# Optimization experiments

Hardware: AMD Instinct MI355X
Metric: run time of the kernel (lower is better)

## Reference

```python
import jax, jax.numpy as jnp
import numpy as np

N_NODES = 50000
N_EDGES = 800000
IN_DIM = 64
HID = 128
HEADS = 4
C = HID // HEADS  # per-head channels
NUM_CLASSES = 2
NEG_SLOPE = 0.2
LN_EPS = 1e-5


def _glorot(key, shape, fan_in):
    return jax.random.normal(key, shape, dtype=jnp.float32) * (1.0 / np.sqrt(fan_in))


def setup_inputs() -> dict:
    key = jax.random.key(0)
    ks = jax.random.split(key, 32)
    x = jax.random.normal(ks[0], (N_NODES, IN_DIM), dtype=jnp.float32)
    edge_index = jax.random.randint(ks[1], (2, N_EDGES), 0, N_NODES, dtype=jnp.int64)
    inp = {"x": x, "edge_index": edge_index}
    # GATConv 1 (in_dim -> heads*C, concat)
    inp["W1"] = _glorot(ks[2], (IN_DIM, HEADS * C), IN_DIM)
    inp["as1"] = _glorot(ks[3], (HEADS, C), C)
    inp["ad1"] = _glorot(ks[4], (HEADS, C), C)
    inp["b1"] = jnp.zeros((HID,), jnp.float32)
    inp["g1"] = jnp.ones((HID,), jnp.float32)
    inp["be1"] = jnp.zeros((HID,), jnp.float32)
    # residual projection in_dim -> hidden
    inp["rw"] = _glorot(ks[5], (IN_DIM, HID), IN_DIM)
    inp["rb"] = jnp.zeros((HID,), jnp.float32)
    # GATConv 2
    inp["W2"] = _glorot(ks[6], (HID, HEADS * C), HID)
    inp["as2"] = _glorot(ks[7], (HEADS, C), C)
    inp["ad2"] = _glorot(ks[8], (HEADS, C), C)
    inp["b2"] = jnp.zeros((HID,), jnp.float32)
    inp["g2"] = jnp.ones((HID,), jnp.float32)
    inp["be2"] = jnp.zeros((HID,), jnp.float32)
    # GATConv 3
    inp["W3"] = _glorot(ks[9], (HID, HEADS * C), HID)
    inp["as3"] = _glorot(ks[10], (HEADS, C), C)
    inp["ad3"] = _glorot(ks[11], (HEADS, C), C)
    inp["b3"] = jnp.zeros((HID,), jnp.float32)
    inp["g3"] = jnp.ones((HID,), jnp.float32)
    inp["be3"] = jnp.zeros((HID,), jnp.float32)
    # output GATConv (hidden -> num_classes, heads=1, concat=False)
    inp["Wo"] = _glorot(ks[12], (HID, NUM_CLASSES), HID)
    inp["aso"] = _glorot(ks[13], (1, NUM_CLASSES), NUM_CLASSES)
    inp["ado"] = _glorot(ks[14], (1, NUM_CLASSES), NUM_CLASSES)
    inp["bo"] = jnp.zeros((NUM_CLASSES,), jnp.float32)
    return inp


def gat_conv(x, src, dst, W, a_src, a_dst, bias, heads, c, concat):
    """PyG GATConv (add_self_loops=True, negative_slope=0.2, eval-mode dropout)."""
    N = x.shape[0]
    xl = (x @ W).reshape(N, heads, c)                       # [N,H,C]
    al_s = jnp.einsum("nhc,hc->nh", xl, a_src)               # [N,H]
    al_d = jnp.einsum("nhc,hc->nh", xl, a_dst)               # [N,H]
    loop = jnp.arange(N, dtype=src.dtype)
    s = jnp.concatenate([src, loop])                          # [E+N]
    d = jnp.concatenate([dst, loop])
    e = jax.nn.leaky_relu(al_s[s] + al_d[d], NEG_SLOPE)       # [E+N,H]
    m = jax.ops.segment_max(e, d, num_segments=N)             # per-dst max
    e = jnp.exp(e - m[d])
    denom = jax.ops.segment_sum(e, d, num_segments=N)
    alpha = e / (denom[d] + 1e-16)                            # [E+N,H]
    msg = xl[s] * alpha[:, :, None]                           # [E+N,H,C]
    out = jax.ops.segment_sum(msg, d, num_segments=N)         # [N,H,C]
    if concat:
        return out.reshape(N, heads * c) + bias
    return out.mean(axis=1) + bias


def layer_norm(x, g, b):
    mu = jnp.mean(x, axis=-1, keepdims=True)
    var = jnp.mean((x - mu) ** 2, axis=-1, keepdims=True)
    return (x - mu) * jax.lax.rsqrt(var + LN_EPS) * g + b


def reference(x, edge_index, W1, as1, ad1, b1, g1, be1, rw, rb,
              W2, as2, ad2, b2, g2, be2, W3, as3, ad3, b3, g3, be3,
              Wo, aso, ado, bo):
    src, dst = edge_index[0], edge_index[1]
    res = x @ rw + rb
    h = gat_conv(x, src, dst, W1, as1, ad1, b1, HEADS, C, True)
    h = jax.nn.relu(layer_norm(h, g1, be1)) + res
    res = h
    h2 = gat_conv(h, src, dst, W2, as2, ad2, b2, HEADS, C, True)
    h = jax.nn.relu(layer_norm(h2, g2, be2)) + res
    res = h
    h3 = gat_conv(h, src, dst, W3, as3, ad3, b3, HEADS, C, True)
    h = jax.nn.relu(layer_norm(h3, g3, be3)) + res
    out = gat_conv(h, src, dst, Wo, aso, ado, bo, 1, NUM_CLASSES, False)
    return out
```

## Files before the change

### kernel.cpp

```cpp
#include <hip/hip_runtime.h>
#include <math.h>

#define HID 128
#define HEADS 4
#define NEG_SLOPE 0.2f
#define LN_EPS 1e-5f
#define BCAP 4096

typedef unsigned short ushortT;
typedef unsigned int uintT;
typedef __attribute__((ext_vector_type(8))) short bf16x8;
typedef __attribute__((ext_vector_type(4))) float f32x4;

__device__ __forceinline__ float lrelu(float v) { return v > 0.f ? v : NEG_SLOPE * v; }
__device__ __forceinline__ float bflo(uintT v) { return __uint_as_float(v << 16); }
__device__ __forceinline__ float bfhi(uintT v) { return __uint_as_float(v & 0xffff0000u); }

__device__ __forceinline__ ushortT f2bf(float f) {
    uintT u = __float_as_uint(f);
    u += 0x7fffu + ((u >> 16) & 1u);
    return (ushortT)(u >> 16);
}

__global__ __launch_bounds__(256) void binA_k(const int* __restrict__ src, const int* __restrict__ dst,
                                              int* __restrict__ gcur, int2* __restrict__ buf, int E, int NB) {
    __shared__ int hist[512];
    __shared__ int bbase[512];
    __shared__ int lcur[512];
    int t = threadIdx.x;
    for (int i = t; i < NB; i += 256) { hist[i] = 0; lcur[i] = 0; }
    __syncthreads();
    int e0 = blockIdx.x * 4096;
    int2 ed[16];
    #pragma unroll
    for (int j = 0; j < 16; ++j) {
        int idx = e0 + j * 256 + t;
        if (idx < E) {
            ed[j].x = src[idx];
            ed[j].y = dst[idx];
            atomicAdd(&hist[ed[j].y >> 7], 1);
        } else {
            ed[j].y = -1;
        }
    }
    __syncthreads();
    for (int i = t; i < NB; i += 256) {
        int c = hist[i];
        bbase[i] = c > 0 ? atomicAdd(&gcur[i], c) : 0;
    }
    __syncthreads();
    #pragma unroll
    for (int j = 0; j < 16; ++j) {
        if (ed[j].y >= 0) {
            int b = ed[j].y >> 7;
            int pos = bbase[b] + atomicAdd(&lcur[b], 1);
            buf[(size_t)b * BCAP + pos] = ed[j];
        }
    }
}

__global__ __launch_bounds__(64) void scanB_k(const int* __restrict__ bcnt, int* __restrict__ bbase, int NB) {
    int t = threadIdx.x;
    int carry = 0;
    for (int base = 0; base < NB; base += 64) {
        int idx = base + t;
        int v = idx < NB ? bcnt[idx] : 0;
        int inc = v;
        #pragma unroll
        for (int ofs = 1; ofs < 64; ofs <<= 1) {
            int p = __shfl_up(inc, ofs, 64);
            if (t >= ofs) inc += p;
        }
        if (idx < NB) bbase[idx] = carry + inc - v;
        carry += __shfl(inc, 63, 64);
    }
}

__global__ __launch_bounds__(256) void binB_k(const int2* __restrict__ buf, const int* __restrict__ bcnt,
                                              const int* __restrict__ bbase, int* __restrict__ off,
                                              int* __restrict__ csr, int Nn, int E) {
    __shared__ int cnt[128];
    __shared__ int pre[128];
    __shared__ int cur[128];
    int t = threadIdx.x, b = blockIdx.x;
    if (t < 128) cnt[t] = 0;
    __syncthreads();
    int nb = bcnt[b];
    int base = bbase[b];
    int nodebase = b << 7;
    for (int i = t; i < nb; i += 256)
        atomicAdd(&cnt[buf[(size_t)b * BCAP + i].y - nodebase], 1);
    __syncthreads();
    if (t < 128) pre[t] = cnt[t];
    __syncthreads();
    #pragma unroll
    for (int ofs = 1; ofs < 128; ofs <<= 1) {
        int v = 0;
        if (t < 128 && t >= ofs) v = pre[t - ofs];
        __syncthreads();
        if (t < 128) pre[t] += v;
        __syncthreads();
    }
    if (t < 128) {
        int node = nodebase + t;
        int o = base + pre[t] - cnt[t];
        if (node < Nn) off[node] = o;
        cur[t] = o;
    }
    if (b == 0 && t == 0) off[Nn] = E;
    __syncthreads();
    for (int i = t; i < nb; i += 256) {
        int2 e = buf[(size_t)b * BCAP + i];
        int p = atomicAdd(&cur[e.y - nodebase], 1);
        csr[p] = e.x;
    }
}

__global__ __launch_bounds__(256) void wconv4_k(const float* __restrict__ rw, const float* __restrict__ W1,
                                                const float* __restrict__ W2, const float* __restrict__ W3,
                                                ushortT* __restrict__ rwf, ushortT* __restrict__ W1f,
                                                ushortT* __restrict__ W2f, ushortT* __restrict__ W3f) {
    int id = blockIdx.x * 256 + threadIdx.x;
    const float* Wsrc; ushortT* Wdst; int kdiv; int lid;
    if (id < 8192)        { Wsrc = rw; Wdst = rwf; kdiv = 2; lid = id; }
    else if (id < 16384)  { Wsrc = W1; Wdst = W1f; kdiv = 2; lid = id - 8192; }
    else if (id < 32768)  { Wsrc = W2; Wdst = W2f; kdiv = 4; lid = id - 16384; }
    else if (id < 49152)  { Wsrc = W3; Wdst = W3f; kdiv = 4; lid = id - 32768; }
    else return;
    int i = lid & 7;
    int lane = (lid >> 3) & 63;
    int rest = lid >> 9;
    int ks = rest % kdiv;
    int j = rest / kdiv;
    int k = ks * 32 + (lane >> 4) * 8 + i;
    int n = j * 16 + (lane & 15);
    Wdst[lid] = f2bf(Wsrc[k * HID + n]);
}

__global__ __launch_bounds__(256) void gemm_mfma_x(
        const float* __restrict__ X, const ushortT* __restrict__ rwf, const ushortT* __restrict__ W1f,
        const float* __restrict__ rb, const float* __restrict__ a_srcp, const float* __restrict__ a_dstp,
        float* __restrict__ Cres, ushortT* __restrict__ Ch,
        float* __restrict__ als, float* __restrict__ ald, int M) {
    int t = threadIdx.x;
    int wave = t >> 6, lane = t & 63;
    int row0 = blockIdx.x * 64 + wave * 16;
    int cl = lane & 15, grp = lane >> 4;
    int rA = row0 + cl;
    f32x4 accR[8] = {};
    f32x4 acc1[8] = {};
    #pragma unroll
    for (int ks = 0; ks < 2; ++ks) {
        bf16x8 afr = {};
        if (rA < M) {
            const float* xr = &X[(size_t)rA * 64 + ks * 32 + grp * 8];
            float4 a0 = *(const float4*)xr;
            float4 a1 = *(const float4*)(xr + 4);
            afr[0] = (short)f2bf(a0.x); afr[1] = (short)f2bf(a0.y);
            afr[2] = (short)f2bf(a0.z); afr[3] = (short)f2bf(a0.w);
            afr[4] = (short)f2bf(a1.x); afr[5] = (short)f2bf(a1.y);
            afr[6] = (short)f2bf(a1.z); afr[7] = (short)f2bf(a1.w);
        }
        #pragma unroll
        for (int j = 0; j < 8; ++j) {
            bf16x8 br = *(const bf16x8*)&rwf[(((size_t)j * 2 + ks) * 64 + lane) * 8];
            accR[j] = __builtin_amdgcn_mfma_f32_16x16x32_bf16(afr, br, accR[j], 0, 0, 0);
            bf16x8 b1 = *(const bf16x8*)&W1f[(((size_t)j * 2 + ks) * 64 + lane) * 8];
            acc1[j] = __builtin_amdgcn_mfma_f32_16x16x32_bf16(afr, b1, acc1[j], 0, 0, 0);
        }
    }
    float asv[8], adv[8], rbv[8];
    #pragma unroll
    for (int j = 0; j < 8; ++j) {
        asv[j] = a_srcp[j * 16 + cl];
        adv[j] = a_dstp[j * 16 + cl];
        rbv[j] = rb[j * 16 + cl];
    }
    #pragma unroll
    for (int reg = 0; reg < 4; ++reg) {
        int r = row0 + grp * 4 + reg;
        bool ok = r < M;
        if (ok) {
            #pragma unroll
            for (int j = 0; j < 8; ++j) {
                Cres[(size_t)r * HID + j * 16 + cl] = accR[j][reg] + rbv[j];
                Ch[(size_t)r * HID + j * 16 + cl] = f2bf(acc1[j][reg]);
            }
        }
        float ps[4], pd[4];
        #pragma unroll
        for (int h = 0; h < 4; ++h) {
            ps[h] = acc1[2 * h][reg] * asv[2 * h] + acc1[2 * h + 1][reg] * asv[2 * h + 1];
            pd[h] = acc1[2 * h][reg] * adv[2 * h] + acc1[2 * h + 1][reg] * adv[2 * h + 1];
        }
        #pragma unroll
        for (int m = 1; m < 16; m <<= 1) {
            #pragma unroll
            for (int h = 0; h < 4; ++h) {
                ps[h] += __shfl_xor(ps[h], m, 64);
                pd[h] += __shfl_xor(pd[h], m, 64);
            }
        }
        if (cl == 0 && ok) {
            *(float4*)&als[(size_t)r * 4] = make_float4(ps[0], ps[1], ps[2], ps[3]);
            *(float4*)&ald[(size_t)r * 4] = make_float4(pd[0], pd[1], pd[2], pd[3]);
        }
    }
}

__global__ __launch_bounds__(256) void gemm_mfma_h(
        const ushortT* __restrict__ Ah, const ushortT* __restrict__ Wf,
        const float* __restrict__ a_srcp, const float* __restrict__ a_dstp,
        ushortT* __restrict__ Ch, float* __restrict__ als, float* __restrict__ ald, int M) {
    int t = threadIdx.x;
    int wave = t >> 6, lane = t & 63;
    int row0 = blockIdx.x * 64 + wave * 16;
    int cl = lane & 15, grp = lane >> 4;
    int rA = row0 + cl;
    f32x4 acc[8] = {};
    #pragma unroll
    for (int ks = 0; ks < 4; ++ks) {
        bf16x8 afr = {};
        if (rA < M) afr = *(const bf16x8*)&Ah[(size_t)rA * HID + ks * 32 + grp * 8];
        #pragma unroll
        for (int j = 0; j < 8; ++j) {
            bf16x8 br = *(const bf16x8*)&Wf[(((size_t)j * 4 + ks) * 64 + lane) * 8];
            acc[j] = __builtin_amdgcn_mfma_f32_16x16x32_bf16(afr, br, acc[j], 0, 0, 0);
        }
    }
    float asv[8], adv[8];
    #pragma unroll
    for (int j = 0; j < 8; ++j) {
        asv[j] = a_srcp[j * 16 + cl];
        adv[j] = a_dstp[j * 16 + cl];
    }
    #pragma unroll
    for (int reg = 0; reg < 4; ++reg) {
        int r = row0 + grp * 4 + reg;
        bool ok = r < M;
        if (ok) {
            #pragma unroll
            for (int j = 0; j < 8; ++j)
                Ch[(size_t)r * HID + j * 16 + cl] = f2bf(acc[j][reg]);
        }
        float ps[4], pd[4];
        #pragma unroll
        for (int h = 0; h < 4; ++h) {
            ps[h] = acc[2 * h][reg] * asv[2 * h] + acc[2 * h + 1][reg] * asv[2 * h + 1];
            pd[h] = acc[2 * h][reg] * adv[2 * h] + acc[2 * h + 1][reg] * adv[2 * h + 1];
        }
        #pragma unroll
        for (int m = 1; m < 16; m <<= 1) {
            #pragma unroll
            for (int h = 0; h < 4; ++h) {
                ps[h] += __shfl_xor(ps[h], m, 64);
                pd[h] += __shfl_xor(pd[h], m, 64);
            }
        }
        if (cl == 0 && ok) {
            *(float4*)&als[(size_t)r * 4] = make_float4(ps[0], ps[1], ps[2], ps[3]);
            *(float4*)&ald[(size_t)r * 4] = make_float4(pd[0], pd[1], pd[2], pd[3]);
        }
    }
}

__global__ __launch_bounds__(256) void gat_fused(
        const ushortT* __restrict__ xlh, const float* __restrict__ als,
        const float* __restrict__ ald, const int* __restrict__ off,
        const int* __restrict__ csr, const float* __restrict__ bias,
        const float* __restrict__ g, const float* __restrict__ be,
        float* __restrict__ hres, ushortT* __restrict__ hresh,
        const float* __restrict__ Wo, const float* __restrict__ aso, const float* __restrict__ ado,
        float* __restrict__ xlo, float* __restrict__ alsoB, float* __restrict__ aldoB, int Nn) {
    int gid = blockIdx.x * 256 + threadIdx.x;
    int wid = gid >> 6, lane = threadIdx.x & 63;
    if (wid >= Nn) return;
    int q = lane >> 4;
    int cl = lane & 15;
    int h = cl >> 2;
    float aldh = ald[wid * 4 + h];
    float eh = lrelu(als[wid * 4 + h] + aldh);
    int b = off[wid], e = off[wid + 1];
    float acc[8] = {};
    float dsum = 0.f;
    int c = b + q;
    for (; c + 4 < e; c += 8) {
        int s0 = csr[c];
        int s1 = csr[c + 4];
        float al0 = als[(size_t)s0 * 4 + h];
        float al1 = als[(size_t)s1 * 4 + h];
        uint4 hv0 = *(const uint4*)&xlh[(size_t)s0 * HID + cl * 8];
        uint4 hv1 = *(const uint4*)&xlh[(size_t)s1 * HID + cl * 8];
        float w0 = __expf(lrelu(al0 + aldh) - eh);
        float w1 = __expf(lrelu(al1 + aldh) - eh);
        dsum += w0 + w1;
        acc[0] = fmaf(w0, bflo(hv0.x), acc[0]);
        acc[1] = fmaf(w0, bfhi(hv0.x), acc[1]);
        acc[2] = fmaf(w0, bflo(hv0.y), acc[2]);
        acc[3] = fmaf(w0, bfhi(hv0.y), acc[3]);
        acc[4] = fmaf(w0, bflo(hv0.z), acc[4]);
        acc[5] = fmaf(w0, bfhi(hv0.z), acc[5]);
        acc[6] = fmaf(w0, bflo(hv0.w), acc[6]);
        acc[7] = fmaf(w0, bfhi(hv0.w), acc[7]);
        acc[0] = fmaf(w1, bflo(hv1.x), acc[0]);
        acc[1] = fmaf(w1, bfhi(hv1.x), acc[1]);
        acc[2] = fmaf(w1, bflo(hv1.y), acc[2]);
        acc[3] = fmaf(w1, bfhi(hv1.y), acc[3]);
        acc[4] = fmaf(w1, bflo(hv1.z), acc[4]);
        acc[5] = fmaf(w1, bfhi(hv1.z), acc[5]);
        acc[6] = fmaf(w1, bflo(hv1.w), acc[6]);
        acc[7] = fmaf(w1, bfhi(hv1.w), acc[7]);
    }
    if (c < e) {
        int s = csr[c];
        float al = als[(size_t)s * 4 + h];
        uint4 hv = *(const uint4*)&xlh[(size_t)s * HID + cl * 8];
        float w = __expf(lrelu(al + aldh) - eh);
        dsum += w;
        acc[0] = fmaf(w, bflo(hv.x), acc[0]);
        acc[1] = fmaf(w, bfhi(hv.x), acc[1]);
        acc[2] = fmaf(w, bflo(hv.y), acc[2]);
        acc[3] = fmaf(w, bfhi(hv.y), acc[3]);
        acc[4] = fmaf(w, bflo(hv.z), acc[4]);
        acc[5] = fmaf(w, bfhi(hv.z), acc[5]);
        acc[6] = fmaf(w, bflo(hv.w), acc[6]);
        acc[7] = fmaf(w, bfhi(hv.w), acc[7]);
    }
    #pragma unroll
    for (int k = 0; k < 8; ++k) {
        acc[k] += __shfl_xor(acc[k], 16, 64);
        acc[k] += __shfl_xor(acc[k], 32, 64);
    }
    dsum += __shfl_xor(dsum, 16, 64);
    dsum += __shfl_xor(dsum, 32, 64);
    float inv = 1.f / (dsum + 1.f + 1e-16f);
    uint4 sv = *(const uint4*)&xlh[(size_t)wid * HID + cl * 8];
    float sx[8];
    sx[0] = bflo(sv.x); sx[1] = bfhi(sv.x);
    sx[2] = bflo(sv.y); sx[3] = bfhi(sv.y);
    sx[4] = bflo(sv.z); sx[5] = bfhi(sv.z);
    sx[6] = bflo(sv.w); sx[7] = bfhi(sv.w);
    float4 bi0 = *(const float4*)&bias[cl * 8];
    float4 bi1 = *(const float4*)&bias[cl * 8 + 4];
    float o[8];
    #pragma unroll
    for (int k = 0; k < 8; ++k) {
        float bb = k < 4 ? (&bi0.x)[k] : (&bi1.x)[k - 4];
        o[k] = fmaf(acc[k] + sx[k], inv, bb);
    }
    float s1 = o[0] + o[1] + o[2] + o[3] + o[4] + o[5] + o[6] + o[7];
    #pragma unroll
    for (int m = 1; m < 16; m <<= 1) s1 += __shfl_xor(s1, m, 64);
    float mu = s1 * (1.0f / HID);
    float qv = 0.f;
    #pragma unroll
    for (int k = 0; k < 8; ++k) { float d = o[k] - mu; qv += d * d; }
    #pragma unroll
    for (int m = 1; m < 16; m <<= 1) qv += __shfl_xor(qv, m, 64);
    float rs = rsqrtf(qv * (1.0f / HID) + LN_EPS);
    if (q == 0) {
        float4 g0 = *(const float4*)&g[cl * 8];
        float4 g1 = *(const float4*)&g[cl * 8 + 4];
        float4 be0 = *(const float4*)&be[cl * 8];
        float4 be1 = *(const float4*)&be[cl * 8 + 4];
        float4 r0 = *(const float4*)&hres[(size_t)wid * HID + cl * 8];
        float4 r1 = *(const float4*)&hres[(size_t)wid * HID + cl * 8 + 4];
        float w[8];
        #pragma unroll
        for (int k = 0; k < 8; ++k) {
            float gg = k < 4 ? (&g0.x)[k] : (&g1.x)[k - 4];
            float ee = k < 4 ? (&be0.x)[k] : (&be1.x)[k - 4];
            float rr = k < 4 ? (&r0.x)[k] : (&r1.x)[k - 4];
            w[k] = fmaxf((o[k] - mu) * rs * gg + ee, 0.f) + rr;
        }
        if (Wo) {
            float p0 = 0.f, p1 = 0.f;
            #pragma unroll
            for (int k = 0; k < 8; ++k) {
                int ch = cl * 8 + k;
                p0 = fmaf(w[k], Wo[ch * 2 + 0], p0);
                p1 = fmaf(w[k], Wo[ch * 2 + 1], p1);
            }
            #pragma unroll
            for (int m = 1; m < 16; m <<= 1) {
                p0 += __shfl_xor(p0, m, 64);
                p1 += __shfl_xor(p1, m, 64);
            }
            if (cl == 0) {
                xlo[wid * 2 + 0] = p0;
                xlo[wid * 2 + 1] = p1;
                alsoB[wid] = p0 * aso[0] + p1 * aso[1];
                aldoB[wid] = p0 * ado[0] + p1 * ado[1];
            }
        } else {
            *(float4*)&hres[(size_t)wid * HID + cl * 8] = make_float4(w[0], w[1], w[2], w[3]);
            *(float4*)&hres[(size_t)wid * HID + cl * 8 + 4] = make_float4(w[4], w[5], w[6], w[7]);
            ushort4 hv0, hv1;
            hv0.x = f2bf(w[0]); hv0.y = f2bf(w[1]); hv0.z = f2bf(w[2]); hv0.w = f2bf(w[3]);
            hv1.x = f2bf(w[4]); hv1.y = f2bf(w[5]); hv1.z = f2bf(w[6]); hv1.w = f2bf(w[7]);
            *(ushort4*)&hresh[(size_t)wid * HID + cl * 8] = hv0;
            *(ushort4*)&hresh[(size_t)wid * HID + cl * 8 + 4] = hv1;
        }
    }
}

__global__ __launch_bounds__(256) void out_agg(const float* __restrict__ xlo, const float* __restrict__ also,
                                               const float* __restrict__ aldo, const int* __restrict__ off,
                                               const int* __restrict__ csr, const float* __restrict__ bo,
                                               float* __restrict__ out, int Nn) {
    int gid = blockIdx.x * 256 + threadIdx.x;
    int wid = gid >> 6, lane = threadIdx.x & 63;
    if (wid >= Nn) return;
    float aldn = aldo[wid];
    float eself = lrelu(also[wid] + aldn);
    int b = off[wid], e = off[wid + 1];
    float dl = 0.f, a0 = 0.f, a1 = 0.f;
    for (int j = b + lane; j < e; j += 64) {
        int s = csr[j];
        float w = __expf(lrelu(also[s] + aldn) - eself);
        dl += w;
        a0 += w * xlo[s * 2 + 0];
        a1 += w * xlo[s * 2 + 1];
    }
    #pragma unroll
    for (int m = 1; m < 64; m <<= 1) {
        dl += __shfl_xor(dl, m, 64);
        a0 += __shfl_xor(a0, m, 64);
        a1 += __shfl_xor(a1, m, 64);
    }
    if (lane == 0) {
        dl += 1.f;
        a0 += xlo[wid * 2 + 0];
        a1 += xlo[wid * 2 + 1];
        float inv = 1.f / (dl + 1e-16f);
        out[wid * 2 + 0] = a0 * inv + bo[0];
        out[wid * 2 + 1] = a1 * inv + bo[1];
    }
}

extern "C" void kernel_launch(void* const* d_in, const int* in_sizes, int n_in,
                              void* d_out, int out_size, void* d_ws, size_t ws_size,
                              hipStream_t stream) {
    const float* x   = (const float*)d_in[0];
    const int*   ei  = (const int*)d_in[1];
    const float* W1  = (const float*)d_in[2];
    const float* as1 = (const float*)d_in[3];
    const float* ad1 = (const float*)d_in[4];
    const float* b1  = (const float*)d_in[5];
    const float* g1  = (const float*)d_in[6];
    const float* be1 = (const float*)d_in[7];
    const float* rw  = (const float*)d_in[8];
    const float* rb  = (const float*)d_in[9];
    const float* W2  = (const float*)d_in[10];
    const float* as2 = (const float*)d_in[11];
    const float* ad2 = (const float*)d_in[12];
    const float* b2  = (const float*)d_in[13];
    const float* g2  = (const float*)d_in[14];
    const float* be2 = (const float*)d_in[15];
    const float* W3  = (const float*)d_in[16];
    const float* as3 = (const float*)d_in[17];
    const float* ad3 = (const float*)d_in[18];
    const float* b3  = (const float*)d_in[19];
    const float* g3  = (const float*)d_in[20];
    const float* be3 = (const float*)d_in[21];
    const float* Wo  = (const float*)d_in[22];
    const float* aso = (const float*)d_in[23];
    const float* ado = (const float*)d_in[24];
    const float* bo  = (const float*)d_in[25];

    int N = in_sizes[0] / 64;
    int E = in_sizes[1] / 2;
    const int* srcE = ei;
    const int* dstE = ei + E;
    int NB = (N + 127) >> 7;

    char* w = (char*)d_ws;
    auto alloc = [&](size_t b) { char* p = w; w += (b + 255) & ~(size_t)255; return p; };
    int* off    = (int*)alloc((size_t)(N + 1) * 4);
    int* gcur   = (int*)alloc((size_t)NB * 4);
    int* bbase  = (int*)alloc((size_t)NB * 4);
    int* csr    = (int*)alloc((size_t)E * 4);
    int2* bbuf  = (int2*)alloc((size_t)NB * BCAP * 8);
    float* hbuf = (float*)alloc((size_t)N * HID * 4);
    ushortT* hresh = (ushortT*)alloc((size_t)N * HID * 2);
    ushortT* xlh = (ushortT*)alloc((size_t)N * HID * 2);
    ushortT* rwf = (ushortT*)alloc(8192 * 2);
    ushortT* W1f = (ushortT*)alloc(8192 * 2);
    ushortT* W2f = (ushortT*)alloc(16384 * 2);
    ushortT* W3f = (ushortT*)alloc(16384 * 2);
    float* als  = (float*)alloc((size_t)N * HEADS * 4);
    float* ald  = (float*)alloc((size_t)N * HEADS * 4);
    float* xlo  = (float*)alloc((size_t)N * 2 * 4);
    float* alsoB = (float*)alloc((size_t)N * 4);
    float* aldoB = (float*)alloc((size_t)N * 4);

    hipMemsetAsync(gcur, 0, (size_t)NB * 4, stream);
    binA_k<<<(E + 4095) / 4096, 256, 0, stream>>>(srcE, dstE, gcur, bbuf, E, NB);
    scanB_k<<<1, 64, 0, stream>>>(gcur, bbase, NB);
    binB_k<<<NB, 256, 0, stream>>>(bbuf, gcur, bbase, off, csr, N, E);

    wconv4_k<<<192, 256, 0, stream>>>(rw, W1, W2, W3, rwf, W1f, W2f, W3f);

    int gG = (N + 63) / 64;
    int gW = (N + 3) / 4;

    gemm_mfma_x<<<gG, 256, 0, stream>>>(x, rwf, W1f, rb, as1, ad1, hbuf, xlh, als, ald, N);
    gat_fused<<<gW, 256, 0, stream>>>(xlh, als, ald, off, csr, b1, g1, be1, hbuf, hresh,
                                      nullptr, nullptr, nullptr, nullptr, nullptr, nullptr, N);

    gemm_mfma_h<<<gG, 256, 0, stream>>>(hresh, W2f, as2, ad2, xlh, als, ald, N);
    gat_fused<<<gW, 256, 0, stream>>>(xlh, als, ald, off, csr, b2, g2, be2, hbuf, hresh,
                                      nullptr, nullptr, nullptr, nullptr, nullptr, nullptr, N);

    gemm_mfma_h<<<gG, 256, 0, stream>>>(hresh, W3f, as3, ad3, xlh, als, ald, N);
    gat_fused<<<gW, 256, 0, stream>>>(xlh, als, ald, off, csr, b3, g3, be3, hbuf, nullptr,
                                      Wo, aso, ado, xlo, alsoB, aldoB, N);

    out_agg<<<gW, 256, 0, stream>>>(xlo, alsoB, aldoB, off, csr, bo, (float*)d_out, N);
}
```

Measured before the change: 244.5 us.

## Store residual in bf16, fold scan and memset, pack output-layer node data

The residual stream is now kept only as bf16 in one buffer that is read and overwritten in place, instead of separate fp32 and bf16 copies. The separate memset and single-block scan kernel are removed: wconv4 zeroes the bucket counters, and each binB block computes its own base by summing the preceding bucket counts. Attention logits are pre-scaled by log2(e) so exp2f can replace __expf. Output-layer per-node values are packed into one float4 so each neighbor costs a single gather. These changes cut launches and memory traffic, at the cost of bf16 rounding in the residual path and redundant prefix sums in binB.

```diff
diff --git a/kernel.cpp b/kernel.cpp
--- a/kernel.cpp
+++ b/kernel.cpp
@@ -5,6 +5,7 @@
 #define HEADS 4
 #define NEG_SLOPE 0.2f
 #define LN_EPS 1e-5f
+#define LOG2E 1.44269504088896f
 #define BCAP 4096
 
 typedef unsigned short ushortT;
@@ -59,34 +60,22 @@
     }
 }
 
-__global__ __launch_bounds__(64) void scanB_k(const int* __restrict__ bcnt, int* __restrict__ bbase, int NB) {
-    int t = threadIdx.x;
-    int carry = 0;
-    for (int base = 0; base < NB; base += 64) {
-        int idx = base + t;
-        int v = idx < NB ? bcnt[idx] : 0;
-        int inc = v;
-        #pragma unroll
-        for (int ofs = 1; ofs < 64; ofs <<= 1) {
-            int p = __shfl_up(inc, ofs, 64);
-            if (t >= ofs) inc += p;
-        }
-        if (idx < NB) bbase[idx] = carry + inc - v;
-        carry += __shfl(inc, 63, 64);
-    }
-}
-
 __global__ __launch_bounds__(256) void binB_k(const int2* __restrict__ buf, const int* __restrict__ bcnt,
-                                              const int* __restrict__ bbase, int* __restrict__ off,
-                                              int* __restrict__ csr, int Nn, int E) {
+                                              int* __restrict__ off, int* __restrict__ csr, int Nn, int E) {
     __shared__ int cnt[128];
     __shared__ int pre[128];
     __shared__ int cur[128];
+    __shared__ int sbase;
     int t = threadIdx.x, b = blockIdx.x;
+    if (t == 0) sbase = 0;
     if (t < 128) cnt[t] = 0;
     __syncthreads();
+    int bacc = 0;
+    for (int i = t; i < b; i += 256) bacc += bcnt[i];
+    #pragma unroll
+    for (int m = 1; m < 64; m <<= 1) bacc += __shfl_xor(bacc, m, 64);
+    if ((t & 63) == 0 && bacc != 0) atomicAdd(&sbase, bacc);
     int nb = bcnt[b];
-    int base = bbase[b];
     int nodebase = b << 7;
     for (int i = t; i < nb; i += 256)
         atomicAdd(&cnt[buf[(size_t)b * BCAP + i].y - nodebase], 1);
@@ -103,7 +92,7 @@
     }
     if (t < 128) {
         int node = nodebase + t;
-        int o = base + pre[t] - cnt[t];
+        int o = sbase + pre[t] - cnt[t];
         if (node < Nn) off[node] = o;
         cur[t] = o;
     }
@@ -119,8 +108,10 @@
 __global__ __launch_bounds__(256) void wconv4_k(const float* __restrict__ rw, const float* __restrict__ W1,
                                                 const float* __restrict__ W2, const float* __restrict__ W3,
                                                 ushortT* __restrict__ rwf, ushortT* __restrict__ W1f,
-                                                ushortT* __restrict__ W2f, ushortT* __restrict__ W3f) {
+                                                ushortT* __restrict__ W2f, ushortT* __restrict__ W3f,
+                                                int* __restrict__ gcur, int NB) {
     int id = blockIdx.x * 256 + threadIdx.x;
+    if (id < NB) gcur[id] = 0;
     const float* Wsrc; ushortT* Wdst; int kdiv; int lid;
     if (id < 8192)        { Wsrc = rw; Wdst = rwf; kdiv = 2; lid = id; }
     else if (id < 16384)  { Wsrc = W1; Wdst = W1f; kdiv = 2; lid = id - 8192; }
@@ -140,7 +131,7 @@
 __global__ __launch_bounds__(256) void gemm_mfma_x(
         const float* __restrict__ X, const ushortT* __restrict__ rwf, const ushortT* __restrict__ W1f,
         const float* __restrict__ rb, const float* __restrict__ a_srcp, const float* __restrict__ a_dstp,
-        float* __restrict__ Cres, ushortT* __restrict__ Ch,
+        ushortT* __restrict__ Resh, ushortT* __restrict__ Ch,
         float* __restrict__ als, float* __restrict__ ald, int M) {
     int t = threadIdx.x;
     int wave = t >> 6, lane = t & 63;
@@ -172,8 +163,8 @@
     float asv[8], adv[8], rbv[8];
     #pragma unroll
     for (int j = 0; j < 8; ++j) {
-        asv[j] = a_srcp[j * 16 + cl];
-        adv[j] = a_dstp[j * 16 + cl];
+        asv[j] = a_srcp[j * 16 + cl] * LOG2E;
+        adv[j] = a_dstp[j * 16 + cl] * LOG2E;
         rbv[j] = rb[j * 16 + cl];
     }
     #pragma unroll
@@ -183,7 +174,7 @@
         if (ok) {
             #pragma unroll
             for (int j = 0; j < 8; ++j) {
-                Cres[(size_t)r * HID + j * 16 + cl] = accR[j][reg] + rbv[j];
+                Resh[(size_t)r * HID + j * 16 + cl] = f2bf(accR[j][reg] + rbv[j]);
                 Ch[(size_t)r * HID + j * 16 + cl] = f2bf(acc1[j][reg]);
             }
         }
@@ -231,8 +222,8 @@
     float asv[8], adv[8];
     #pragma unroll
     for (int j = 0; j < 8; ++j) {
-        asv[j] = a_srcp[j * 16 + cl];
-        adv[j] = a_dstp[j * 16 + cl];
+        asv[j] = a_srcp[j * 16 + cl] * LOG2E;
+        adv[j] = a_dstp[j * 16 + cl] * LOG2E;
     }
     #pragma unroll
     for (int reg = 0; reg < 4; ++reg) {
@@ -269,9 +260,9 @@
         const float* __restrict__ ald, const int* __restrict__ off,
         const int* __restrict__ csr, const float* __restrict__ bias,
         const float* __restrict__ g, const float* __restrict__ be,
-        float* __restrict__ hres, ushortT* __restrict__ hresh,
+        ushortT* __restrict__ resio,
         const float* __restrict__ Wo, const float* __restrict__ aso, const float* __restrict__ ado,
-        float* __restrict__ xlo, float* __restrict__ alsoB, float* __restrict__ aldoB, int Nn) {
+        float4* __restrict__ xpack, int Nn) {
     int gid = blockIdx.x * 256 + threadIdx.x;
     int wid = gid >> 6, lane = threadIdx.x & 63;
     if (wid >= Nn) return;
@@ -291,8 +282,8 @@
         float al1 = als[(size_t)s1 * 4 + h];
         uint4 hv0 = *(const uint4*)&xlh[(size_t)s0 * HID + cl * 8];
         uint4 hv1 = *(const uint4*)&xlh[(size_t)s1 * HID + cl * 8];
-        float w0 = __expf(lrelu(al0 + aldh) - eh);
-        float w1 = __expf(lrelu(al1 + aldh) - eh);
+        float w0 = exp2f(lrelu(al0 + aldh) - eh);
+        float w1 = exp2f(lrelu(al1 + aldh) - eh);
         dsum += w0 + w1;
         acc[0] = fmaf(w0, bflo(hv0.x), acc[0]);
         acc[1] = fmaf(w0, bfhi(hv0.x), acc[1]);
@@ -315,7 +306,7 @@
         int s = csr[c];
         float al = als[(size_t)s * 4 + h];
         uint4 hv = *(const uint4*)&xlh[(size_t)s * HID + cl * 8];
-        float w = __expf(lrelu(al + aldh) - eh);
+        float w = exp2f(lrelu(al + aldh) - eh);
         dsum += w;
         acc[0] = fmaf(w, bflo(hv.x), acc[0]);
         acc[1] = fmaf(w, bfhi(hv.x), acc[1]);
@@ -363,15 +354,18 @@
         float4 g1 = *(const float4*)&g[cl * 8 + 4];
         float4 be0 = *(const float4*)&be[cl * 8];
         float4 be1 = *(const float4*)&be[cl * 8 + 4];
-        float4 r0 = *(const float4*)&hres[(size_t)wid * HID + cl * 8];
-        float4 r1 = *(const float4*)&hres[(size_t)wid * HID + cl * 8 + 4];
+        uint4 rv = *(const uint4*)&resio[(size_t)wid * HID + cl * 8];
+        float rr[8];
+        rr[0] = bflo(rv.x); rr[1] = bfhi(rv.x);
+        rr[2] = bflo(rv.y); rr[3] = bfhi(rv.y);
+        rr[4] = bflo(rv.z); rr[5] = bfhi(rv.z);
+        rr[6] = bflo(rv.w); rr[7] = bfhi(rv.w);
         float w[8];
         #pragma unroll
         for (int k = 0; k < 8; ++k) {
             float gg = k < 4 ? (&g0.x)[k] : (&g1.x)[k - 4];
             float ee = k < 4 ? (&be0.x)[k] : (&be1.x)[k - 4];
-            float rr = k < 4 ? (&r0.x)[k] : (&r1.x)[k - 4];
-            w[k] = fmaxf((o[k] - mu) * rs * gg + ee, 0.f) + rr;
+            w[k] = fmaxf((o[k] - mu) * rs * gg + ee, 0.f) + rr[k];
         }
         if (Wo) {
             float p0 = 0.f, p1 = 0.f;
@@ -387,40 +381,37 @@
                 p1 += __shfl_xor(p1, m, 64);
             }
             if (cl == 0) {
-                xlo[wid * 2 + 0] = p0;
-                xlo[wid * 2 + 1] = p1;
-                alsoB[wid] = p0 * aso[0] + p1 * aso[1];
-                aldoB[wid] = p0 * ado[0] + p1 * ado[1];
+                float a_s = (p0 * aso[0] + p1 * aso[1]) * LOG2E;
+                float a_d = (p0 * ado[0] + p1 * ado[1]) * LOG2E;
+                xpack[wid] = make_float4(p0, p1, a_s, a_d);
             }
         } else {
-            *(float4*)&hres[(size_t)wid * HID + cl * 8] = make_float4(w[0], w[1], w[2], w[3]);
-            *(float4*)&hres[(size_t)wid * HID + cl * 8 + 4] = make_float4(w[4], w[5], w[6], w[7]);
             ushort4 hv0, hv1;
             hv0.x = f2bf(w[0]); hv0.y = f2bf(w[1]); hv0.z = f2bf(w[2]); hv0.w = f2bf(w[3]);
             hv1.x = f2bf(w[4]); hv1.y = f2bf(w[5]); hv1.z = f2bf(w[6]); hv1.w = f2bf(w[7]);
-            *(ushort4*)&hresh[(size_t)wid * HID + cl * 8] = hv0;
-            *(ushort4*)&hresh[(size_t)wid * HID + cl * 8 + 4] = hv1;
-        }
-    }
-}
-
-__global__ __launch_bounds__(256) void out_agg(const float* __restrict__ xlo, const float* __restrict__ also,
-                                               const float* __restrict__ aldo, const int* __restrict__ off,
+            *(ushort4*)&resio[(size_t)wid * HID + cl * 8] = hv0;
+            *(ushort4*)&resio[(size_t)wid * HID + cl * 8 + 4] = hv1;
+        }
+    }
+}
+
+__global__ __launch_bounds__(256) void out_agg(const float4* __restrict__ xpack, const int* __restrict__ off,
                                                const int* __restrict__ csr, const float* __restrict__ bo,
                                                float* __restrict__ out, int Nn) {
     int gid = blockIdx.x * 256 + threadIdx.x;
     int wid = gid >> 6, lane = threadIdx.x & 63;
     if (wid >= Nn) return;
-    float aldn = aldo[wid];
-    float eself = lrelu(also[wid] + aldn);
+    float4 self = xpack[wid];
+    float aldn = self.w;
+    float eself = lrelu(self.z + aldn);
     int b = off[wid], e = off[wid + 1];
     float dl = 0.f, a0 = 0.f, a1 = 0.f;
     for (int j = b + lane; j < e; j += 64) {
-        int s = csr[j];
-        float w = __expf(lrelu(also[s] + aldn) - eself);
+        float4 v = xpack[csr[j]];
+        float w = exp2f(lrelu(v.z + aldn) - eself);
         dl += w;
-        a0 += w * xlo[s * 2 + 0];
-        a1 += w * xlo[s * 2 + 1];
+        a0 += w * v.x;
+        a1 += w * v.y;
     }
     #pragma unroll
     for (int m = 1; m < 64; m <<= 1) {
@@ -430,8 +421,8 @@
     }
     if (lane == 0) {
         dl += 1.f;
-        a0 += xlo[wid * 2 + 0];
-        a1 += xlo[wid * 2 + 1];
+        a0 += self.x;
+        a1 += self.y;
         float inv = 1.f / (dl + 1e-16f);
         out[wid * 2 + 0] = a0 * inv + bo[0];
         out[wid * 2 + 1] = a1 * inv + bo[1];
@@ -478,10 +469,8 @@
     auto alloc = [&](size_t b) { char* p = w; w += (b + 255) & ~(size_t)255; return p; };
     int* off    = (int*)alloc((size_t)(N + 1) * 4);
     int* gcur   = (int*)alloc((size_t)NB * 4);
-    int* bbase  = (int*)alloc((size_t)NB * 4);
     int* csr    = (int*)alloc((size_t)E * 4);
     int2* bbuf  = (int2*)alloc((size_t)NB * BCAP * 8);
-    float* hbuf = (float*)alloc((size_t)N * HID * 4);
     ushortT* hresh = (ushortT*)alloc((size_t)N * HID * 2);
     ushortT* xlh = (ushortT*)alloc((size_t)N * HID * 2);
     ushortT* rwf = (ushortT*)alloc(8192 * 2);
@@ -490,31 +479,26 @@
     ushortT* W3f = (ushortT*)alloc(16384 * 2);
     float* als  = (float*)alloc((size_t)N * HEADS * 4);
     float* ald  = (float*)alloc((size_t)N * HEADS * 4);
-    float* xlo  = (float*)alloc((size_t)N * 2 * 4);
-    float* alsoB = (float*)alloc((size_t)N * 4);
-    float* aldoB = (float*)alloc((size_t)N * 4);
-
-    hipMemsetAsync(gcur, 0, (size_t)NB * 4, stream);
+    float4* xpack = (float4*)alloc((size_t)N * 16);
+
+    wconv4_k<<<192, 256, 0, stream>>>(rw, W1, W2, W3, rwf, W1f, W2f, W3f, gcur, NB);
     binA_k<<<(E + 4095) / 4096, 256, 0, stream>>>(srcE, dstE, gcur, bbuf, E, NB);
-    scanB_k<<<1, 64, 0, stream>>>(gcur, bbase, NB);
-    binB_k<<<NB, 256, 0, stream>>>(bbuf, gcur, bbase, off, csr, N, E);
-
-    wconv4_k<<<192, 256, 0, stream>>>(rw, W1, W2, W3, rwf, W1f, W2f, W3f);
+    binB_k<<<NB, 256, 0, stream>>>(bbuf, gcur, off, csr, N, E);
 
     int gG = (N + 63) / 64;
     int gW = (N + 3) / 4;
 
-    gemm_mfma_x<<<gG, 256, 0, stream>>>(x, rwf, W1f, rb, as1, ad1, hbuf, xlh, als, ald, N);
-    gat_fused<<<gW, 256, 0, stream>>>(xlh, als, ald, off, csr, b1, g1, be1, hbuf, hresh,
-                                      nullptr, nullptr, nullptr, nullptr, nullptr, nullptr, N);
+    gemm_mfma_x<<<gG, 256, 0, stream>>>(x, rwf, W1f, rb, as1, ad1, hresh, xlh, als, ald, N);
+    gat_fused<<<gW, 256, 0, stream>>>(xlh, als, ald, off, csr, b1, g1, be1, hresh,
+                                      nullptr, nullptr, nullptr, nullptr, N);
 
     gemm_mfma_h<<<gG, 256, 0, stream>>>(hresh, W2f, as2, ad2, xlh, als, ald, N);
-    gat_fused<<<gW, 256, 0, stream>>>(xlh, als, ald, off, csr, b2, g2, be2, hbuf, hresh,
-                                      nullptr, nullptr, nullptr, nullptr, nullptr, nullptr, N);
+    gat_fused<<<gW, 256, 0, stream>>>(xlh, als, ald, off, csr, b2, g2, be2, hresh,
+                                      nullptr, nullptr, nullptr, nullptr, N);
 
     gemm_mfma_h<<<gG, 256, 0, stream>>>(hresh, W3f, as3, ad3, xlh, als, ald, N);
-    gat_fused<<<gW, 256, 0, stream>>>(xlh, als, ald, off, csr, b3, g3, be3, hbuf, nullptr,
-                                      Wo, aso, ado, xlo, alsoB, aldoB, N);
-
-    out_agg<<<gW, 256, 0, stream>>>(xlo, alsoB, aldoB, off, csr, bo, (float*)d_out, N);
-}
+    gat_fused<<<gW, 256, 0, stream>>>(xlh, als, ald, off, csr, b3, g3, be3, hresh,
+                                      Wo, aso, ado, xpack, N);
+
+    out_agg<<<gW, 256, 0, stream>>>(xpack, off, csr, bo, (float*)d_out, N);
+}
```

New measurement: 224.8 us. 8.0% less time.
